# Kernel optimization log

Hardware: AMD Instinct MI355X
Metric: run time of the kernel (lower is better)

The kernel has to match this reference:

```python
import jax, jax.numpy as jnp
import numpy as np

B, N, M, D = 128, 4096, 64, 16
SQRT_D = 4
SCALE = 1.0 / (D ** 0.5)
LN_EPS = 1e-5


def setup_inputs() -> dict:
    key = jax.random.key(0)
    k1, k2, k3 = jax.random.split(key, 3)
    w_const = np.sqrt(M / (SQRT_D * N)).astype(np.float32)
    return {
        "input": jax.random.normal(k1, (B, N, D), dtype=jnp.float32),
        "next_capsule_value": jax.random.normal(k2, (B, M, D), dtype=jnp.float32),
        "w": w_const * jax.random.normal(k3, (N, SQRT_D, SQRT_D, M), dtype=jnp.float32),
        "ln_w": jnp.ones((D,), dtype=jnp.float32),
        "ln_b": jnp.zeros((D,), dtype=jnp.float32),
        "num_iter": 1,
    }


def reference(input, next_capsule_value, w, ln_w, ln_b, num_iter):
    b = input.shape[0]
    # matrix-pose view: [B, N, sqrt_d, sqrt_d] and [B, M, sqrt_d, sqrt_d]
    x = input.reshape(b, N, SQRT_D, SQRT_D)
    ncv = next_capsule_value.reshape(b, M, SQRT_D, SQRT_D)
    # QK-like routing scores: [B, N, M]
    qk = jnp.einsum('bnax,nxdm,bmad->bnm', x, w, ncv) * SCALE
    qk = jax.nn.softmax(qk, axis=2)
    qk = qk / (jnp.sum(qk, axis=2, keepdims=True) + 1e-10)
    # weighted aggregation -> [B, M, sqrt_d, sqrt_d] -> [B, M, D]
    out = jnp.einsum('bnm,bnax,nxdm->bmad', qk, x, w).reshape(b, M, D)
    # dropout rate = 0.0 -> identity; LayerNorm over last dim
    mu = jnp.mean(out, axis=-1, keepdims=True)
    var = jnp.var(out, axis=-1, keepdims=True)
    out = (out - mu) * jax.lax.rsqrt(var + LN_EPS) * ln_w + ln_b
    return out
```

## Files before the change

kernel.cpp:

```cpp
#include <hip/hip_runtime.h>
#include <stdint.h>

#define B_ 128
#define N_ 4096
#define M_ 64
#define D_ 16
#define SCALE_ 0.25f
#define NSLICE 128
#define SLICE_N 32
#define OUT_ELEMS (B_ * M_ * D_)

template<int CTRL, int RM, int BC>
__device__ __forceinline__ float dpp_f(float old, float src) {
  return __int_as_float(__builtin_amdgcn_update_dpp(
      __float_as_int(old), __float_as_int(src), CTRL, RM, 0xF, BC));
}

__device__ __forceinline__ float wave_sum64(float x) {
  x += dpp_f<0x121, 0xF, 1>(0.f, x);
  x += dpp_f<0x122, 0xF, 1>(0.f, x);
  x += dpp_f<0x124, 0xF, 1>(0.f, x);
  x += dpp_f<0x128, 0xF, 1>(0.f, x);
  x += dpp_f<0x142, 0xA, 1>(0.f, x);
  x += dpp_f<0x143, 0xC, 1>(0.f, x);
  return __int_as_float(__builtin_amdgcn_readlane(__float_as_int(x), 63));
}

template<int EPI>
__global__ __launch_bounds__(256, 4)
void capsule_main(const float* __restrict__ x_in, const float* __restrict__ ncv_in,
                  const float* __restrict__ w_in, float* __restrict__ dst) {
  const int L     = blockIdx.x;
  const int bg    = L >> 7;
  const int inner = L & 127;
  const int s     = ((inner & 7) << 4) | (inner >> 3);
  const int lane  = threadIdx.x & 63;
  const int wid   = __builtin_amdgcn_readfirstlane((int)(threadIdx.x >> 6));
  const int t     = threadIdx.x;
  const int b0    = bg * 8 + wid * 2;
  const int n0    = s * SLICE_N;

  __shared__ float xls[8 * SLICE_N * D_];

#pragma unroll
  for (int k = 0; k < 4; ++k) {
    const int g  = t + 256 * k;
    const int b8 = g >> 7;
    const int rem = g & 127;
    ((float4*)xls)[g] =
        ((const float4*)x_in)[((size_t)(bg * 8 + b8) * N_ + n0) * 4 + rem];
  }

  float ncv[2][16];
#pragma unroll
  for (int bb = 0; bb < 2; ++bb) {
    const float4* p = (const float4*)(ncv_in + ((size_t)(b0 + bb) * M_ + lane) * D_);
#pragma unroll
    for (int q = 0; q < 4; ++q) {
      float4 v = p[q];
      ncv[bb][q*4+0] = v.x; ncv[bb][q*4+1] = v.y;
      ncv[bb][q*4+2] = v.z; ncv[bb][q*4+3] = v.w;
    }
  }

  float acc[2][16];
#pragma unroll
  for (int bb = 0; bb < 2; ++bb)
#pragma unroll
    for (int j = 0; j < 16; ++j) acc[bb][j] = 0.f;

  __syncthreads();

  const float* wp = w_in + (size_t)n0 * 1024 + lane;

#pragma unroll 2
  for (int i = 0; i < SLICE_N; ++i) {
    float wv[16];
#pragma unroll
    for (int xd = 0; xd < 16; ++xd) wv[xd] = wp[(size_t)i * 1024 + xd * 64];

#pragma unroll
    for (int bb = 0; bb < 2; ++bb) {
      const float4* xp4 = (const float4*)&xls[((wid * 2 + bb) * SLICE_N + i) * D_];
      float xv[16];
#pragma unroll
      for (int q = 0; q < 4; ++q) {
        float4 v = xp4[q];
        xv[q*4+0] = v.x; xv[q*4+1] = v.y; xv[q*4+2] = v.z; xv[q*4+3] = v.w;
      }
      float vote[16];
#pragma unroll
      for (int a = 0; a < 4; ++a) {
#pragma unroll
        for (int d = 0; d < 4; ++d) {
          float v = xv[a*4+0] * wv[0*4+d];
          v = fmaf(xv[a*4+1], wv[1*4+d], v);
          v = fmaf(xv[a*4+2], wv[2*4+d], v);
          v = fmaf(xv[a*4+3], wv[3*4+d], v);
          vote[a*4+d] = v;
        }
      }
      float q0 = 0.f, q1 = 0.f, q2 = 0.f, q3 = 0.f;
#pragma unroll
      for (int j = 0; j < 4; ++j) {
        q0 = fmaf(vote[j],      ncv[bb][j],      q0);
        q1 = fmaf(vote[4 + j],  ncv[bb][4 + j],  q1);
        q2 = fmaf(vote[8 + j],  ncv[bb][8 + j],  q2);
        q3 = fmaf(vote[12 + j], ncv[bb][12 + j], q3);
      }
      const float sc = ((q0 + q1) + (q2 + q3)) * SCALE_;
      const float p  = __expf(sc);
      const float sm = wave_sum64(p);
      const float rr = p / sm;
#pragma unroll
      for (int j = 0; j < 16; ++j) acc[bb][j] = fmaf(rr, vote[j], acc[bb][j]);
    }
  }

  if (EPI == 1) {
#pragma unroll
    for (int bb = 0; bb < 2; ++bb) {
      float4* op = (float4*)(dst + ((size_t)(s * B_ + b0 + bb) * M_ + lane) * D_);
#pragma unroll
      for (int q = 0; q < 4; ++q) {
        float4 v;
        v.x = acc[bb][q*4+0]; v.y = acc[bb][q*4+1];
        v.z = acc[bb][q*4+2]; v.w = acc[bb][q*4+3];
        op[q] = v;
      }
    }
  } else {
#pragma unroll
    for (int bb = 0; bb < 2; ++bb) {
      float* op = dst + ((size_t)(b0 + bb) * M_ + lane) * D_;
#pragma unroll
      for (int j = 0; j < 16; ++j) atomicAdd(op + j, acc[bb][j]);
    }
  }
}

__global__ void reduce_ln(const float* __restrict__ ws, float* __restrict__ out,
                          const float* __restrict__ lw, const float* __restrict__ lb) {
  const int t = blockIdx.x * 256 + threadIdx.x;
  const float* p = ws + t;
  float sacc = 0.f;
#pragma unroll 8
  for (int sl = 0; sl < NSLICE; ++sl) sacc += p[(size_t)sl * OUT_ELEMS];
  float sv = sacc;
#pragma unroll
  for (int m = 1; m < 16; m <<= 1) sv += __shfl_xor(sv, m, 16);
  const float mu = sv * 0.0625f;
  const float dv = sacc - mu;
  float s2 = dv * dv;
#pragma unroll
  for (int m = 1; m < 16; m <<= 1) s2 += __shfl_xor(s2, m, 16);
  out[t] = dv * rsqrtf(s2 * 0.0625f + 1e-5f) * lw[t & 15] + lb[t & 15];
}

__global__ void capsule_ln(float* __restrict__ out, const float* __restrict__ lw,
                           const float* __restrict__ lb) {
  const int t = blockIdx.x * 256 + threadIdx.x;
  const float v = out[t];
  float sv = v;
#pragma unroll
  for (int m = 1; m < 16; m <<= 1) sv += __shfl_xor(sv, m, 16);
  const float mu = sv * 0.0625f;
  const float dv = v - mu;
  float s2 = dv * dv;
#pragma unroll
  for (int m = 1; m < 16; m <<= 1) s2 += __shfl_xor(s2, m, 16);
  out[t] = dv * rsqrtf(s2 * 0.0625f + 1e-5f) * lw[t & 15] + lb[t & 15];
}

extern "C" void kernel_launch(void* const* d_in, const int* in_sizes, int n_in,
                              void* d_out, int out_size, void* d_ws, size_t ws_size,
                              hipStream_t stream) {
  (void)in_sizes; (void)n_in; (void)out_size;
  const float* x_in = (const float*)d_in[0];
  const float* ncv  = (const float*)d_in[1];
  const float* w    = (const float*)d_in[2];
  const float* lw   = (const float*)d_in[3];
  const float* lb   = (const float*)d_in[4];
  float* out = (float*)d_out;

  const size_t need = (size_t)NSLICE * OUT_ELEMS * sizeof(float);
  if (ws_size >= need) {
    float* ws = (float*)d_ws;
    capsule_main<1><<<2048, 256, 0, stream>>>(x_in, ncv, w, ws);
    reduce_ln<<<OUT_ELEMS / 256, 256, 0, stream>>>(ws, out, lw, lb);
  } else {
    hipMemsetAsync(out, 0, sizeof(float) * OUT_ELEMS, stream);
    capsule_main<0><<<2048, 256, 0, stream>>>(x_in, ncv, w, out);
    capsule_ln<<<OUT_ELEMS / 256, 256, 0, stream>>>(out, lw, lb);
  }
}
```

Before: 205.1 us.

## Split slice reduction into two-stage float4 kernels and use exp2/rcp in softmax

The slice-reduction-plus-LayerNorm kernel, which had too few threads each striding over 128 slices, is replaced by a two-stage reduction. The first kernel runs 512 blocks, each summing a group of 32 slices with float4 loads. The second sums the four partials and applies LayerNorm with float4 vectors and 4-lane shuffles. The main kernel folds the score scale and log2(e) into the preloaded ncv values, uses a hardware exp2, and replaces the division with a fast reciprocal. This trades a little precision and one extra kernel launch for more parallelism and less ALU work.

```diff
diff --git a/kernel.cpp b/kernel.cpp
--- a/kernel.cpp
+++ b/kernel.cpp
@@ -5,10 +5,16 @@
 #define N_ 4096
 #define M_ 64
 #define D_ 16
-#define SCALE_ 0.25f
 #define NSLICE 128
 #define SLICE_N 32
 #define OUT_ELEMS (B_ * M_ * D_)
+#define OUT4 (OUT_ELEMS / 4)
+
+#if __has_builtin(__builtin_amdgcn_exp2f)
+#define EXP2F(x) __builtin_amdgcn_exp2f(x)
+#else
+#define EXP2F(x) __expf((x) * 0.69314718f)
+#endif
 
 template<int CTRL, int RM, int BC>
 __device__ __forceinline__ float dpp_f(float old, float src) {
@@ -44,13 +50,14 @@
 
 #pragma unroll
   for (int k = 0; k < 4; ++k) {
-    const int g  = t + 256 * k;
-    const int b8 = g >> 7;
+    const int g   = t + 256 * k;
+    const int b8  = g >> 7;
     const int rem = g & 127;
     ((float4*)xls)[g] =
         ((const float4*)x_in)[((size_t)(bg * 8 + b8) * N_ + n0) * 4 + rem];
   }
 
+  const float QS = 0.25f * 1.44269504f;
   float ncv[2][16];
 #pragma unroll
   for (int bb = 0; bb < 2; ++bb) {
@@ -58,8 +65,8 @@
 #pragma unroll
     for (int q = 0; q < 4; ++q) {
       float4 v = p[q];
-      ncv[bb][q*4+0] = v.x; ncv[bb][q*4+1] = v.y;
-      ncv[bb][q*4+2] = v.z; ncv[bb][q*4+3] = v.w;
+      ncv[bb][q*4+0] = v.x * QS; ncv[bb][q*4+1] = v.y * QS;
+      ncv[bb][q*4+2] = v.z * QS; ncv[bb][q*4+3] = v.w * QS;
     }
   }
 
@@ -108,10 +115,10 @@
         q2 = fmaf(vote[8 + j],  ncv[bb][8 + j],  q2);
         q3 = fmaf(vote[12 + j], ncv[bb][12 + j], q3);
       }
-      const float sc = ((q0 + q1) + (q2 + q3)) * SCALE_;
-      const float p  = __expf(sc);
+      const float sc = (q0 + q1) + (q2 + q3);
+      const float p  = EXP2F(sc);
       const float sm = wave_sum64(p);
-      const float rr = p / sm;
+      const float rr = p * __builtin_amdgcn_rcpf(sm);
 #pragma unroll
       for (int j = 0; j < 16; ++j) acc[bb][j] = fmaf(rr, vote[j], acc[bb][j]);
     }
@@ -139,22 +146,50 @@
   }
 }
 
-__global__ void reduce_ln(const float* __restrict__ ws, float* __restrict__ out,
-                          const float* __restrict__ lw, const float* __restrict__ lb) {
-  const int t = blockIdx.x * 256 + threadIdx.x;
-  const float* p = ws + t;
-  float sacc = 0.f;
-#pragma unroll 8
-  for (int sl = 0; sl < NSLICE; ++sl) sacc += p[(size_t)sl * OUT_ELEMS];
-  float sv = sacc;
-#pragma unroll
-  for (int m = 1; m < 16; m <<= 1) sv += __shfl_xor(sv, m, 16);
+__global__ void reduce_part(float4* __restrict__ ws4) {
+  const int blk = blockIdx.x;
+  const int sg  = blk >> 7;
+  const int f   = ((blk & 127) << 8) + threadIdx.x;
+  const size_t base = (size_t)(sg * 32) * OUT4 + f;
+  float4 s0 = ws4[base];
+  float4 s1 = ws4[base + OUT4];
+#pragma unroll 4
+  for (int k = 2; k < 32; k += 2) {
+    float4 a = ws4[base + (size_t)k * OUT4];
+    float4 b = ws4[base + (size_t)(k + 1) * OUT4];
+    s0.x += a.x; s0.y += a.y; s0.z += a.z; s0.w += a.w;
+    s1.x += b.x; s1.y += b.y; s1.z += b.z; s1.w += b.w;
+  }
+  float4 r;
+  r.x = s0.x + s1.x; r.y = s0.y + s1.y; r.z = s0.z + s1.z; r.w = s0.w + s1.w;
+  ws4[base] = r;
+}
+
+__global__ void reduce_ln2(const float4* __restrict__ ws4, float4* __restrict__ out4,
+                           const float* __restrict__ lw, const float* __restrict__ lb) {
+  const int f = blockIdx.x * 256 + threadIdx.x;
+  float4 s = ws4[f];
+#pragma unroll
+  for (int sg = 1; sg < 4; ++sg) {
+    float4 a = ws4[(size_t)(sg * 32) * OUT4 + f];
+    s.x += a.x; s.y += a.y; s.z += a.z; s.w += a.w;
+  }
+  float sv = (s.x + s.y) + (s.z + s.w);
+  sv += __shfl_xor(sv, 1, 4);
+  sv += __shfl_xor(sv, 2, 4);
   const float mu = sv * 0.0625f;
-  const float dv = sacc - mu;
-  float s2 = dv * dv;
-#pragma unroll
-  for (int m = 1; m < 16; m <<= 1) s2 += __shfl_xor(s2, m, 16);
-  out[t] = dv * rsqrtf(s2 * 0.0625f + 1e-5f) * lw[t & 15] + lb[t & 15];
+  float4 d;
+  d.x = s.x - mu; d.y = s.y - mu; d.z = s.z - mu; d.w = s.w - mu;
+  float s2 = (d.x*d.x + d.y*d.y) + (d.z*d.z + d.w*d.w);
+  s2 += __shfl_xor(s2, 1, 4);
+  s2 += __shfl_xor(s2, 2, 4);
+  const float inv = rsqrtf(s2 * 0.0625f + 1e-5f);
+  const float4 w4 = ((const float4*)lw)[f & 3];
+  const float4 b4 = ((const float4*)lb)[f & 3];
+  float4 o;
+  o.x = d.x * inv * w4.x + b4.x; o.y = d.y * inv * w4.y + b4.y;
+  o.z = d.z * inv * w4.z + b4.z; o.w = d.w * inv * w4.w + b4.w;
+  out4[f] = o;
 }
 
 __global__ void capsule_ln(float* __restrict__ out, const float* __restrict__ lw,
@@ -187,7 +222,8 @@
   if (ws_size >= need) {
     float* ws = (float*)d_ws;
     capsule_main<1><<<2048, 256, 0, stream>>>(x_in, ncv, w, ws);
-    reduce_ln<<<OUT_ELEMS / 256, 256, 0, stream>>>(ws, out, lw, lb);
+    reduce_part<<<512, 256, 0, stream>>>((float4*)ws);
+    reduce_ln2<<<OUT4 / 256, 256, 0, stream>>>((const float4*)ws, (float4*)out, lw, lb);
   } else {
     hipMemsetAsync(out, 0, sizeof(float) * OUT_ELEMS, stream);
     capsule_main<0><<<2048, 256, 0, stream>>>(x_in, ncv, w, out);
```

After: 197.9 us. 3.5% less time.
